# Kernel tuning notes

Measured on AMD Instinct MI355X. Metric: run time of the kernel, lower is better.

Reference implementation:

```python
import jax, jax.numpy as jnp
import numpy as np

B = 128; N_PER = 64; E_UND = 256
N_TOT = B * N_PER; E_DIR = 2 * B * E_UND; E_KEEP = B * E_UND
F_IN = 5; H1 = 256; H2 = 512; ATT = 3 * H2
EPS = 1e-5


def setup_inputs() -> dict:
    rng = np.random.default_rng(0)
    # undirected edges within each graph, stored in both directions
    u = rng.integers(0, N_PER, size=(B, E_UND))
    v = (u + rng.integers(1, N_PER, size=(B, E_UND))) % N_PER
    base = np.arange(B)[:, None] * N_PER
    lo = np.minimum(u, v) + base
    hi = np.maximum(u, v) + base
    edges = np.stack([np.concatenate([lo, hi], 1).reshape(-1),
                      np.concatenate([hi, lo], 1).reshape(-1)])
    ea = np.stack([rng.random(E_DIR).astype(np.float32),
                   rng.integers(0, 2, E_DIR).astype(np.float32)], axis=1)
    key = jax.random.key(0)
    ks = iter(jax.random.split(key, 16))
    lin = lambda i, o: jax.random.normal(next(ks), (i, o), jnp.float32) * 0.02
    return dict(
        x=jax.random.normal(next(ks), (N_TOT, F_IN), jnp.float32),
        edges=jnp.asarray(edges, jnp.int32),
        edge_attr=jnp.asarray(ea),
        detector_labels=jnp.ones((N_TOT,), bool),
        batch_labels=jnp.repeat(jnp.arange(B, dtype=jnp.int32), N_PER),
        w_emb_W=lin(3, 1), w_emb_b=jnp.zeros((1,), jnp.float32),
        gc1_Wrel=lin(F_IN, H1), gc1_brel=jnp.zeros((H1,)), gc1_Wroot=lin(F_IN, H1),
        gc2_Wrel=lin(H1, H2), gc2_brel=jnp.zeros((H2,)), gc2_Wroot=lin(H1, H2),
        gn_w=jnp.ones((H2,)), gn_b=jnp.zeros((H2,)), gn_ms=jnp.ones((H2,)),
        edge_emb_W=lin(3, H2), edge_emb_b=jnp.zeros((H2,)),
        qkv_W=lin(ATT, 3 * ATT), qkv_b=jnp.zeros((3 * ATT,)),
        in_Wq=lin(ATT, ATT), in_Wk=lin(ATT, ATT), in_Wv=lin(ATT, ATT),
        in_bq=jnp.zeros((ATT,)), in_bk=jnp.zeros((ATT,)), in_bv=jnp.zeros((ATT,)),
        out_W=lin(ATT, ATT), out_b=jnp.zeros((ATT,)),
        ln_g=jnp.ones((ATT,)), ln_b=jnp.zeros((ATT,)),
        head_W=lin(ATT, 1), head_b=jnp.zeros((1,)),
    )


def reference(x, edges, edge_attr, detector_labels, batch_labels,
              w_emb_W, w_emb_b, gc1_Wrel, gc1_brel, gc1_Wroot,
              gc2_Wrel, gc2_brel, gc2_Wroot, gn_w, gn_b, gn_ms,
              edge_emb_W, edge_emb_b, qkv_W, qkv_b,
              in_Wq, in_Wk, in_Wv, in_bq, in_bk, in_bv,
              out_W, out_b, ln_g, ln_b, head_W, head_b):
    src, dst = edges[0], edges[1]
    onehot = lambda c: jax.nn.one_hot(jax.lax.stop_gradient(c).astype(jnp.int32), 2, dtype=x.dtype)
    # edge-weight embedding
    w = jnp.concatenate([edge_attr[:, :1], onehot(edge_attr[:, 1])], axis=-1)
    w = jax.nn.relu(w @ w_emb_W + w_emb_b)  # [E_DIR, 1]

    def gconv(h, Wrel, brel, Wroot):  # torch_geometric GraphConv (aggr='add')
        agg = jax.ops.segment_sum(w * h[src], dst, num_segments=N_TOT)
        return jax.nn.relu(agg @ Wrel + brel + h @ Wroot)

    h = gconv(x, gc1_Wrel, gc1_brel, gc1_Wroot)
    h = gconv(h, gc2_Wrel, gc2_brel, gc2_Wroot)
    # GraphNorm: per-graph statistics
    cnt = jax.ops.segment_sum(jnp.ones((N_TOT, 1), h.dtype), batch_labels, num_segments=B)
    mean = jax.ops.segment_sum(h, batch_labels, num_segments=B) / cnt
    cen = h - gn_ms * mean[batch_labels]
    var = jax.ops.segment_sum(cen * cen, batch_labels, num_segments=B) / cnt
    h = gn_w * cen / jnp.sqrt(var + EPS)[batch_labels] + gn_b
    # SplitSyndromes: keep detector-detector edges with src > dst, then sort (row-major)
    keep = detector_labels[src] & detector_labels[dst] & (src > dst)
    kidx = jnp.nonzero(keep, size=E_KEEP)[0]  # E_KEEP known by construction
    e_src, e_dst, ea = src[kidx], dst[kidx], edge_attr[kidx]
    perm = jnp.argsort(e_src * N_TOT + e_dst)
    e_src, e_dst, ea = e_src[perm], e_dst[perm], ea[perm]
    emb = jax.nn.relu(jnp.concatenate([ea[:, :1], onehot(ea[:, 1])], -1) @ edge_emb_W + edge_emb_b)
    feat = jnp.concatenate([h[e_src], emb, h[e_dst]], axis=-1)  # [E_KEEP, ATT]
    # equal edge count per graph => unbatch + pad_sequence == reshape
    feat = feat.reshape(B, E_UND, ATT)
    se = e_src.reshape(B, E_UND); te = e_dst.reshape(B, E_UND)
    ec = ea[:, 1].reshape(B, E_UND, 1)
    mask = se == te  # key_padding_mask (all False: no padding here)
    # self-attention, 1 head
    q, k, v = jnp.split(feat @ qkv_W + qkv_b, 3, axis=-1)
    q = q @ in_Wq + in_bq; k = k @ in_Wk + in_bk; v = v @ in_Wv + in_bv
    scale = np.float32(1.0 / np.sqrt(ATT))
    scores = jnp.einsum('bqd,bkd->bqk', q, k) * scale
    scores = jnp.where(mask[:, None, :], -jnp.inf, scores)
    attn_out = jnp.einsum('bqk,bkd->bqd', jax.nn.softmax(scores, axis=-1), v) @ out_W + out_b
    feat = feat + attn_out
    mu = feat.mean(-1, keepdims=True)
    feat = ln_g * (feat - mu) * jax.lax.rsqrt(((feat - mu) ** 2).mean(-1, keepdims=True) + EPS) + ln_b
    out = feat @ head_W + head_b  # [B, E_UND, 1]
    pair = jnp.concatenate([out[:, ::2], out[:, 1::2]], axis=2)  # [B, E_UND/2, 2]
    ecp = jnp.concatenate([ec[:, ::2], ec[:, 1::2]], axis=2)
    min_inds = jnp.argmin(pair, axis=2, keepdims=True)
    val = jnp.take_along_axis(pair, min_inds, axis=2)
    cls = jnp.take_along_axis(ecp, min_inds, axis=2)
    edges_out = jnp.stack([se, te], axis=-1)[:, ::2, :]
    return edges_out, val, cls
```

## Files before the change

kernel.cpp:

```cpp
#include <hip/hip_runtime.h>
#include <math.h>

#define NTOT   8192
#define BGR    128
#define NPER   64
#define EDIR   65536
#define EKEEP  32768
#define EPSC   1e-5f

typedef unsigned short ushortT;
typedef __attribute__((ext_vector_type(8))) short bf16x8;
typedef __attribute__((ext_vector_type(4))) float f32x4;

#define C_BF 0
#define C_F32 1
#define C_RT 2

__device__ __forceinline__ float bf2f(ushortT u) {
    union { unsigned int i; float f; } v; v.i = ((unsigned int)u) << 16; return v.f;
}
__device__ __forceinline__ ushortT f2bf(float f) {
    unsigned int u = __float_as_uint(f);
    u += 0x7FFFu + ((u >> 16) & 1u);
    return (ushortT)(u >> 16);
}
__device__ __forceinline__ float get1(const void* p, long i, int f) {
    return f ? ((const float*)p)[i] : bf2f(((const ushortT*)p)[i]);
}
__device__ __forceinline__ float ld1c(const float* p)   { return *p; }
__device__ __forceinline__ float ld1c(const ushortT* p) { return bf2f(*p); }
__device__ __forceinline__ void st1c(float* p, float v)   { *p = v; }
__device__ __forceinline__ void st1c(ushortT* p, float v) { *p = f2bf(v); }
__device__ __forceinline__ int clampi(int v, int lo, int hi) {
    return v < lo ? lo : (v > hi ? hi : v);
}

__device__ __forceinline__ void gld16(const void* g, void* l) {
    __builtin_amdgcn_global_load_lds(
        (const __attribute__((address_space(1))) unsigned int*)g,
        (__attribute__((address_space(3))) unsigned int*)l, 16, 0, 0);
}

__device__ __forceinline__ int xcd_swz(int flat, int nwg) {
    const int q = nwg >> 3, r = nwg & 7;
    const int xcd = flat & 7, idx = flat >> 3;
    return (xcd < r ? xcd * (q + 1) : r * (q + 1) + (xcd - r) * q) + idx;
}

__launch_bounds__(256)
__global__ void detect_k(const unsigned int* __restrict__ xw, int* __restrict__ flag)
{
    __shared__ int red[256];
    const int t = threadIdx.x;
    int hits = 0;
#pragma unroll
    for (int i = 0; i < 4; ++i) {
        const unsigned w = xw[t*4 + i];
        const unsigned eb = (w >> 7) & 0xFF;
        hits += (eb >= 100 && eb <= 150) ? 1 : 0;
    }
    red[t] = hits; __syncthreads();
#pragma unroll
    for (int s = 128; s > 0; s >>= 1) { if (t < s) red[t] += red[t+s]; __syncthreads(); }
    if (t == 0) *flag = (red[0] < 512) ? 1 : 0;
}

template<class TC, bool BIAS, bool RESID, bool RELU>
__launch_bounds__(256)
__global__ void bgemm_k(const ushortT* __restrict__ A, const ushortT* __restrict__ B,
                        const float* __restrict__ bias, TC* __restrict__ C,
                        int K, int lda, int ldb, int ldc,
                        long sA, long sB, long sC, long biasOff, long bzStride,
                        float alpha)
{
    const int t = threadIdx.x;
    const int lane = t & 63, wave = t >> 6;
    const int l15 = lane & 15, quad = lane >> 4;
    const int wr = (wave >> 1) * 64, wc = (wave & 1) * 64;

    const int gx = gridDim.x, gy = gridDim.y;
    const int nwg = gx * gy * (int)gridDim.z;
    const int flat = xcd_swz(blockIdx.x + gx * (blockIdx.y + gy * blockIdx.z), nwg);
    const int bx = flat % gx;
    const int by = (flat / gx) % gy;
    const int bz = flat / (gx * gy);

    const int m0 = by * 128, n0 = bx * 128;
    const long z = bz;

    __shared__ __align__(16) ushortT As[128][64];
    __shared__ __align__(16) ushortT Bs[128][64];

    f32x4 acc[4][4] = {};

    const int sr = t >> 3;
    const int ssw = ((t & 7) ^ (sr & 7)) * 8;
    const ushortT* pA = A + z*sA + (long)(m0 + sr) * lda + ssw;
    const ushortT* pB = B + z*sB + (long)(n0 + sr) * ldb + ssw;
    ushortT* lA = &As[sr][(t & 7) * 8];
    ushortT* lB = &Bs[sr][(t & 7) * 8];

    for (int k0 = 0; k0 < K; k0 += 64) {
#pragma unroll
        for (int i = 0; i < 4; ++i) {
            gld16(pA + (long)i*32*lda + k0, lA + i*32*64);
            gld16(pB + (long)i*32*ldb + k0, lB + i*32*64);
        }
        __syncthreads();
#pragma unroll
        for (int kh = 0; kh < 2; ++kh) {
            const int ca = (kh*32 + quad*8) ^ ((l15 & 7) * 8);
            bf16x8 af[4], bfr[4];
#pragma unroll
            for (int i = 0; i < 4; ++i) {
                af[i]  = *(const bf16x8*)&As[wr + i*16 + l15][ca];
                bfr[i] = *(const bf16x8*)&Bs[wc + i*16 + l15][ca];
            }
#pragma unroll
            for (int mt = 0; mt < 4; ++mt)
#pragma unroll
                for (int nt = 0; nt < 4; ++nt)
                    acc[mt][nt] = __builtin_amdgcn_mfma_f32_16x16x32_bf16(af[mt], bfr[nt], acc[mt][nt], 0, 0, 0);
        }
        __syncthreads();
    }

    TC* Cb = C + z * sC;
#pragma unroll
    for (int nt = 0; nt < 4; ++nt) {
        const int col = n0 + wc + nt*16 + l15;
        const float bv = BIAS ? bias[biasOff + z*bzStride + col] : 0.f;
#pragma unroll
        for (int mt = 0; mt < 4; ++mt) {
#pragma unroll
            for (int r = 0; r < 4; ++r) {
                const int row = m0 + wr + mt*16 + quad*4 + r;
                TC* cp = Cb + (long)row * ldc + col;
                float val = alpha * acc[mt][nt][r] + bv;
                if constexpr (RESID) val += ld1c(cp);
                if constexpr (RELU)  val = fmaxf(val, 0.f);
                st1c(cp, val);
            }
        }
    }
}

__device__ __forceinline__ float blockReduceSum(float v, float* red, int t)
{
    red[t] = v; __syncthreads();
#pragma unroll
    for (int s = 128; s > 0; s >>= 1) {
        if (t < s) red[t] += red[t + s];
        __syncthreads();
    }
    const float r = red[0];
    __syncthreads();
    return r;
}

__launch_bounds__(256)
__global__ void convbf_k(const void* __restrict__ in, ushortT* __restrict__ out,
                         long n4, const int* __restrict__ flagp)
{
    const int f = *flagp;
    const long i = (long)blockIdx.x*256 + threadIdx.x;
    if (i >= n4) return;
    const long i0 = i * 4;
    if (f) {
        const float4 v = *(const float4*)((const float*)in + i0);
        ushort4 o; o.x=f2bf(v.x); o.y=f2bf(v.y); o.z=f2bf(v.z); o.w=f2bf(v.w);
        *(ushort4*)(out + i0) = o;
    } else {
        *(ushort4*)(out + i0) = *(const ushort4*)((const ushortT*)in + i0);
    }
}

__launch_bounds__(256)
__global__ void tconvbf_k(const void* __restrict__ in, ushortT* __restrict__ out,
                          const int* __restrict__ flagp)
{
    const int f = *flagp;
    __shared__ float tile[32][33];
    const int bx = blockIdx.x, by = blockIdx.y;
    const int tx = threadIdx.x & 31, ty = threadIdx.x >> 5;
#pragma unroll
    for (int i = 0; i < 4; ++i) {
        const int k = by*32 + ty + i*8;
        tile[ty + i*8][tx] = get1(in, (long)k*1536 + bx*32 + tx, f);
    }
    __syncthreads();
#pragma unroll
    for (int i = 0; i < 4; ++i) {
        const int n = bx*32 + ty + i*8;
        out[(long)n*1536 + by*32 + tx] = f2bf(tile[tx][ty + i*8]);
    }
}

__launch_bounds__(256)
__global__ void tconv512_k(const void* __restrict__ in, ushortT* __restrict__ out,
                           int koff, const int* __restrict__ flagp)
{
    const int f = *flagp;
    __shared__ float tile[32][33];
    const int bx = blockIdx.x, by = blockIdx.y;
    const int tx = threadIdx.x & 31, ty = threadIdx.x >> 5;
#pragma unroll
    for (int i = 0; i < 4; ++i) {
        const int k = by*32 + ty + i*8;
        tile[ty + i*8][tx] = get1(in, (long)k*512 + bx*32 + tx, f);
    }
    __syncthreads();
#pragma unroll
    for (int i = 0; i < 4; ++i) {
        const int n = bx*32 + ty + i*8;
        out[(long)n*512 + koff + by*32 + tx] = f2bf(tile[tx][ty + i*8]);
    }
}

__launch_bounds__(256)
__global__ void convf32_k(const void* __restrict__ in, float* __restrict__ out,
                          int n, const int* __restrict__ flagp)
{
    const int f = *flagp;
    const int i = blockIdx.x*256 + threadIdx.x;
    if (i < n) out[i] = get1(in, i, f);
}

__launch_bounds__(256)
__global__ void colcomb_part_k(const void* __restrict__ v, int cv, long voff,
                               const void* __restrict__ W, int cW,
                               float* __restrict__ part, const int* __restrict__ flagp)
{
    const int rtf = *flagp;
    const int fv = (cv == C_RT) ? rtf : cv;
    const int fW = (cW == C_RT) ? rtf : cW;
    const int d = blockIdx.x*256 + threadIdx.x;
    const int c0 = blockIdx.y * 24;
    float a = 0.f;
#pragma unroll
    for (int i = 0; i < 24; ++i) {
        const int c = c0 + i;
        a += get1(v, voff + c, fv) * get1(W, (long)c*1536 + d, fW);
    }
    part[blockIdx.y * 1536 + d] = a;
}

__launch_bounds__(256)
__global__ void colcomb_red_k(const float* __restrict__ part,
                              const void* __restrict__ b, int cb,
                              float* __restrict__ out, const int* __restrict__ flagp)
{
    const int rtf = *flagp;
    const int fb = (cb == C_RT) ? rtf : cb;
    const int d = blockIdx.x*256 + threadIdx.x;
    float a = get1(b, d, fb);
#pragma unroll 8
    for (int cy = 0; cy < 64; ++cy) a += part[cy*1536 + d];
    out[d] = a;
}

__launch_bounds__(256)
__global__ void rowdot_k(const ushortT* __restrict__ W, const float* __restrict__ v,
                         float* __restrict__ out, float scale)
{
    const int r = blockIdx.x, t = threadIdx.x;
    __shared__ float red[256];
    float p = 0.f;
    for (int c = t; c < 1536; c += 256) p += bf2f(W[(long)r*1536 + c]) * v[c];
    const float tot = blockReduceSum(p, red, t);
    if (t == 0) out[r] = scale * tot;
}

__launch_bounds__(256)
__global__ void gconv1_k(int b0, const void* __restrict__ x, const int* __restrict__ edges,
                         const void* __restrict__ ea,
                         const void* __restrict__ wembW, const void* __restrict__ wembB,
                         const void* __restrict__ Wrel, const void* __restrict__ brel,
                         const void* __restrict__ Wroot, ushortT* __restrict__ ah,
                         const int* __restrict__ flagp)
{
    const int f = *flagp;
    const int bl = blockIdx.x, g = b0 + bl, t = threadIdx.x;
    __shared__ float s_x[64][5];
    __shared__ float s_agg[64][5];
    __shared__ int   s_cnt[64];
    __shared__ int   s_off[65];
    __shared__ int   s_src[512];
    __shared__ float s_w[512];

    if (t < 64) s_cnt[t] = 0;
    if (t < 320) s_x[t/5][t%5] = get1(x, (long)(g*64 + t/5)*5 + (t%5), f);
    __syncthreads();

    const float w0 = get1(wembW,0,f), w1 = get1(wembW,1,f), w2 = get1(wembW,2,f);
    const float wb = get1(wembB,0,f);
    int sl[2], dl[2], slot[2]; float wv[2];
#pragma unroll
    for (int e2 = 0; e2 < 2; ++e2) {
        const int e = g*512 + t + 256*e2;
        const int s = edges[e], d = edges[EDIR + e];
        sl[e2] = clampi(s - g*64, 0, 63); dl[e2] = clampi(d - g*64, 0, 63);
        const float a0 = get1(ea, 2L*e, f), a1 = get1(ea, 2L*e+1, f);
        wv[e2] = fmaxf(a0*w0 + ((a1 < 0.5f) ? w1 : w2) + wb, 0.f);
        slot[e2] = atomicAdd(&s_cnt[dl[e2]], 1);
    }
    __syncthreads();
    if (t == 0) {
        int r = 0;
        for (int i = 0; i < 64; ++i) { s_off[i] = r; r += s_cnt[i]; }
        s_off[64] = r;
    }
    __syncthreads();
#pragma unroll
    for (int e2 = 0; e2 < 2; ++e2) {
        const int p = s_off[dl[e2]] + slot[e2];
        s_src[p] = sl[e2]; s_w[p] = wv[e2];
    }
    __syncthreads();
    if (t < 320) {
        const int n = t/5, k = t%5;
        float acc = 0.f;
        for (int i = s_off[n]; i < s_off[n+1]; ++i) acc += s_w[i] * s_x[s_src[i]][k];
        s_agg[n][k] = acc;
    }
    __syncthreads();
    float wr[5], wo[5];
#pragma unroll
    for (int k = 0; k < 5; ++k) { wr[k] = get1(Wrel, k*256 + t, f); wo[k] = get1(Wroot, k*256 + t, f); }
    const float bb = get1(brel, t, f);
    for (int n = 0; n < 64; ++n) {
        float v = bb;
#pragma unroll
        for (int k = 0; k < 5; ++k) v += s_agg[n][k]*wr[k] + s_x[n][k]*wo[k];
        ah[(long)(bl*64 + n)*512 + 256 + t] = f2bf(fmaxf(v, 0.f));
    }
}

__launch_bounds__(256)
__global__ void gconv2_agg_k(int b0, ushortT* __restrict__ ah, const int* __restrict__ edges,
                             const void* __restrict__ ea,
                             const void* __restrict__ wembW, const void* __restrict__ wembB,
                             const int* __restrict__ flagp)
{
    const int f = *flagp;
    const int bl = blockIdx.x, g = b0 + bl, t = threadIdx.x;
    __shared__ int   s_cnt[64];
    __shared__ int   s_off[65];
    __shared__ int   s_src[512];
    __shared__ float s_w[512];

    if (t < 64) s_cnt[t] = 0;
    __syncthreads();

    const float w0 = get1(wembW,0,f), w1 = get1(wembW,1,f), w2 = get1(wembW,2,f);
    const float wb = get1(wembB,0,f);
    int sl[2], dl[2], slot[2]; float wv[2];
#pragma unroll
    for (int e2 = 0; e2 < 2; ++e2) {
        const int e = g*512 + t + 256*e2;
        const int s = edges[e], d = edges[EDIR + e];
        sl[e2] = clampi(s - g*64, 0, 63); dl[e2] = clampi(d - g*64, 0, 63);
        const float a0 = get1(ea, 2L*e, f), a1 = get1(ea, 2L*e+1, f);
        wv[e2] = fmaxf(a0*w0 + ((a1 < 0.5f) ? w1 : w2) + wb, 0.f);
        slot[e2] = atomicAdd(&s_cnt[dl[e2]], 1);
    }
    __syncthreads();
    if (t == 0) {
        int r = 0;
        for (int i = 0; i < 64; ++i) { s_off[i] = r; r += s_cnt[i]; }
        s_off[64] = r;
    }
    __syncthreads();
#pragma unroll
    for (int e2 = 0; e2 < 2; ++e2) {
        const int p = s_off[dl[e2]] + slot[e2];
        s_src[p] = sl[e2]; s_w[p] = wv[e2];
    }
    __syncthreads();
    for (int n = 0; n < 64; ++n) {
        float acc = 0.f;
        const int i0 = s_off[n], i1 = s_off[n+1];
        for (int i = i0; i < i1; ++i)
            acc += s_w[i] * bf2f(ah[(long)(bl*64 + s_src[i])*512 + 256 + t]);
        ah[(long)(bl*64 + n)*512 + t] = f2bf(acc);
    }
}

__launch_bounds__(256)
__global__ void gnorm_k(ushortT* __restrict__ h, const void* __restrict__ gw,
                        const void* __restrict__ gb, const void* __restrict__ gms,
                        const int* __restrict__ flagp)
{
    const int f0 = *flagp;
    const int bl = blockIdx.x, t = threadIdx.x;
    const int f = t + 256*blockIdx.y;
    float acc = 0.f;
    for (int n = 0; n < 64; ++n) acc += bf2f(h[(bl*64+n)*512 + f]);
    const float m2 = get1(gms, f, f0) * (acc * (1.f/64.f));
    float v = 0.f;
    for (int n = 0; n < 64; ++n) { const float d = bf2f(h[(bl*64+n)*512 + f]) - m2; v += d*d; }
    const float rs = rsqrtf(v*(1.f/64.f) + EPSC);
    const float g = get1(gw, f, f0), bb = get1(gb, f, f0);
    for (int n = 0; n < 64; ++n) {
        const int idx = (bl*64+n)*512 + f;
        h[idx] = f2bf(g * (bf2f(h[idx]) - m2) * rs + bb);
    }
}

__launch_bounds__(256)
__global__ void sort_k(const int* __restrict__ edges, int* __restrict__ sorted_orig,
                       int* __restrict__ se, int* __restrict__ te)
{
    const int b = blockIdx.x, t = threadIdx.x;
    __shared__ int s_keep[512];
    __shared__ int s_key[512];
    __shared__ int s_ckey[256];
    __shared__ int s_corig[256];
#pragma unroll
    for (int e2 = 0; e2 < 2; ++e2) {
        const int el = t + 256*e2;
        const int e = b*512 + el;
        const int s = edges[e], d = edges[EDIR + e];
        s_keep[el] = (s > d) ? 1 : 0;
        s_key[el]  = ((s - b*64) << 6) | (d - b*64);
    }
    __syncthreads();
#pragma unroll
    for (int e2 = 0; e2 < 2; ++e2) {
        const int el = t + 256*e2;
        if (s_keep[el]) {
            int pos = 0;
            for (int j = 0; j < el; ++j) pos += s_keep[j];
            s_ckey[pos]  = s_key[el];
            s_corig[pos] = b*512 + el;
        }
    }
    __syncthreads();
    const int ki = s_ckey[t];
    int rank = 0;
    for (int j = 0; j < 256; ++j) {
        const int kj = s_ckey[j];
        rank += (kj < ki || (kj == ki && j < t)) ? 1 : 0;
    }
    const int orig = s_corig[t];
    const int p = b*256 + rank;
    sorted_orig[p] = orig;
    se[p] = edges[orig];
    te[p] = edges[EDIR + orig];
}

__launch_bounds__(256)
__global__ void fbuild_k(int b0, int maxn, const ushortT* __restrict__ h,
                         const int* __restrict__ sorted_orig,
                         const int* __restrict__ se, const int* __restrict__ te,
                         const void* __restrict__ ea,
                         const void* __restrict__ eW, const void* __restrict__ eB,
                         const float* __restrict__ kb,
                         ushortT* __restrict__ F, float* __restrict__ bvec,
                         const int* __restrict__ flagp)
{
    const int fl = *flagp;
    const int e = blockIdx.x, t = threadIdx.x;
    __shared__ float red[256];
    const int ge = b0*256 + e;
    const int s = clampi(se[ge] - b0*64, 0, maxn);
    const int d = clampi(te[ge] - b0*64, 0, maxn);
    const int orig = clampi(sorted_orig[ge], 0, EDIR-1);
    const float a0 = get1(ea, 2L*orig, fl), a1 = get1(ea, 2L*orig + 1, fl);
    float partial = 0.f;
#pragma unroll
    for (int c = 0; c < 6; ++c) {
        const int col = c*256 + t;
        float v;
        if (c < 2) {
            v = bf2f(h[(long)s*512 + col]);
        } else if (c < 4) {
            const int ff = col - 512;
            v = fmaxf(a0*get1(eW, ff, fl)
                      + ((a1 < 0.5f) ? get1(eW, 512+ff, fl) : get1(eW, 1024+ff, fl))
                      + get1(eB, ff, fl), 0.f);
        } else {
            v = bf2f(h[(long)d*512 + (col - 1024)]);
        }
        F[(long)e*1536 + col] = f2bf(v);
        partial += v * kb[col];
    }
    const float tot = blockReduceSum(partial, red, t);
    if (t == 0) bvec[ge] = tot;
}

__launch_bounds__(256)
__global__ void softmax_ip_k(float* __restrict__ S)
{
    const long row = blockIdx.x;
    const int t = threadIdx.x;
    __shared__ float red[256];
    const float v = S[row*256 + t];
    red[t] = v; __syncthreads();
#pragma unroll
    for (int s = 128; s > 0; s >>= 1) { if (t < s) red[t] = fmaxf(red[t], red[t+s]); __syncthreads(); }
    const float mx = red[0]; __syncthreads();
    const float e = __expf(v - mx);
    red[t] = e; __syncthreads();
#pragma unroll
    for (int s = 128; s > 0; s >>= 1) { if (t < s) red[t] += red[t+s]; __syncthreads(); }
    const float sum = red[0];
    ((ushortT*)S)[row*512 + t] = f2bf(e / sum);
}

__launch_bounds__(256)
__global__ void ln_head_k(int b0, const ushortT* __restrict__ F, const void* __restrict__ lng,
                          const void* __restrict__ lnb, const void* __restrict__ hW,
                          const void* __restrict__ hB, float* __restrict__ gout,
                          const int* __restrict__ flagp)
{
    const int fl = *flagp;
    const int e = blockIdx.x, t = threadIdx.x;
    __shared__ float red[256];
    float xv[6];
    float s = 0.f;
#pragma unroll
    for (int c = 0; c < 6; ++c) { xv[c] = bf2f(F[(long)e*1536 + c*256 + t]); s += xv[c]; }
    const float tot = blockReduceSum(s, red, t);
    const float mu = tot * (1.f/1536.f);
    float ss = 0.f;
#pragma unroll
    for (int c = 0; c < 6; ++c) { const float d = xv[c] - mu; ss += d*d; }
    const float tot2 = blockReduceSum(ss, red, t);
    const float rs = rsqrtf(tot2 * (1.f/1536.f) + EPSC);
    float p = 0.f;
#pragma unroll
    for (int c = 0; c < 6; ++c) {
        const int col = c*256 + t;
        p += (get1(lng, col, fl) * (xv[c] - mu) * rs + get1(lnb, col, fl)) * get1(hW, col, fl);
    }
    const float tot3 = blockReduceSum(p, red, t);
    if (t == 0) gout[b0*256 + e] = tot3 + get1(hB, 0, fl);
}

__launch_bounds__(128)
__global__ void final_k(const float* __restrict__ gout, const int* __restrict__ se,
                        const int* __restrict__ te, const int* __restrict__ sorted_orig,
                        const void* __restrict__ ea, float* __restrict__ out,
                        const int* __restrict__ flagp)
{
    const int fl = *flagp;
    const int b = blockIdx.x, j = threadIdx.x;
    const int e0 = b*256 + 2*j, e1 = e0 + 1;
    const float p0 = gout[e0], p1 = gout[e1];
    const int idx = (p1 < p0) ? 1 : 0;
    const float val = idx ? p1 : p0;
    const int eo = idx ? e1 : e0;
    const int orig = clampi(sorted_orig[eo], 0, EDIR-1);
    const float cls = get1(ea, 2L*orig + 1, fl);
    out[(b*128 + j)*2 + 0] = (float)se[e0];
    out[(b*128 + j)*2 + 1] = (float)te[e0];
    out[32768 + b*128 + j] = val;
    out[32768 + 16384 + b*128 + j] = cls;
}

extern "C" void kernel_launch(void* const* d_in, const int* in_sizes, int n_in,
                              void* d_out, int out_size, void* d_ws, size_t ws_size,
                              hipStream_t stream)
{
    (void)out_size;

    const void* x     = d_in[0];
    const int*  edges = (const int*)d_in[1];
    const void* ea    = d_in[2];

    int ws0 = 3;
    while (ws0 < n_in && in_sizes[ws0] != 3) ++ws0;
    if (ws0 + 27 > n_in) ws0 = 5;

    const void* wembW  = d_in[ws0 + 0];
    const void* wembB  = d_in[ws0 + 1];
    const void* g1Wrel = d_in[ws0 + 2];
    const void* g1brel = d_in[ws0 + 3];
    const void* g1Wroot= d_in[ws0 + 4];
    const void* g2Wrel = d_in[ws0 + 5];
    const void* g2brel = d_in[ws0 + 6];
    const void* g2Wroot= d_in[ws0 + 7];
    const void* gnw    = d_in[ws0 + 8];
    const void* gnb    = d_in[ws0 + 9];
    const void* gnms   = d_in[ws0 + 10];
    const void* eembW  = d_in[ws0 + 11];
    const void* eembB  = d_in[ws0 + 12];
    const void* qkvW   = d_in[ws0 + 13];
    const void* qkvb   = d_in[ws0 + 14];
    const void* inWq   = d_in[ws0 + 15];
    const void* inWk   = d_in[ws0 + 16];
    const void* inWv   = d_in[ws0 + 17];
    const void* inbq   = d_in[ws0 + 18];
    const void* inbv   = d_in[ws0 + 20];
    const void* outW   = d_in[ws0 + 21];
    const void* outb   = d_in[ws0 + 22];
    const void* lng    = d_in[ws0 + 23];
    const void* lnb    = d_in[ws0 + 24];
    const void* headW  = d_in[ws0 + 25];
    const void* headb  = d_in[ws0 + 26];

    char* ws = (char*)d_ws;
    size_t off = 0;
    auto alloc = [&](size_t bytes) {
        void* p = ws + off;
        off = (off + bytes + 255) & ~(size_t)255;
        return p;
    };
    int*     dflag  = (int*)    alloc(256);
    float*   gout   = (float*)  alloc(EKEEP*4);
    int*     sorted = (int*)    alloc(EKEEP*4);
    int*     seg    = (int*)    alloc(EKEEP*4);
    int*     teg    = (int*)    alloc(EKEEP*4);
    float*   bvec   = (float*)  alloc(EKEEP*4);
    float*   bqc    = (float*)  alloc(1536*4);
    float*   bvc    = (float*)  alloc(1536*4);
    float*   kb     = (float*)  alloc(1536*4);
    float*   bvo    = (float*)  alloc(1536*4);
    float*   g2bf   = (float*)  alloc(512*4);
    float*   colpart= (float*)  alloc(64L*1536*4);
    ushortT* Wg2T   = (ushortT*)alloc(512L*512*2);
    ushortT* MpWv   = (ushortT*)alloc(2L*1536*1536*2);
    ushortT* MpT    = MpWv;
    ushortT* Wvo    = MpWv + 1536L*1536;
    const size_t fixedB = off;

    const long W2 = 1536L * 1536;
    ushortT* Wqc    = (ushortT*)(ws + fixedB);
    ushortT* Wkc    = Wqc + W2;
    ushortT* Wvc    = Wqc + 2*W2;
    ushortT* outWT  = Wqc + 3*W2;
    ushortT* qkvWbf = Wqc + 4*W2;
    ushortT* inWqT  = Wqc + 7*W2;
    ushortT* inWkT  = Wqc + 8*W2;
    ushortT* inWvT  = Wqc + 9*W2;

    const size_t perG = 64L*512*2 + 64L*512*2 + 2L*256*1536*2 + 256L*256*4;
    int G = 128;
    while (G > 2 && fixedB + (size_t)G*perG + 65536 > ws_size) G >>= 1;

    size_t coff = fixedB;
    auto calloc2 = [&](size_t bytes) {
        void* p = ws + coff;
        coff = (coff + bytes + 255) & ~(size_t)255;
        return p;
    };
    ushortT* h_c  = (ushortT*)calloc2((size_t)G*64*512*2);
    ushortT* ah_c = (ushortT*)calloc2((size_t)G*64*512*2);
    ushortT* F_c  = (ushortT*)calloc2((size_t)G*256*1536*2);
    ushortT* T_c  = (ushortT*)calloc2((size_t)G*256*1536*2);
    float*   S_c  = (float*)  calloc2((size_t)G*256*256*4);

    const float scale = 0.02551551815399144f;
    const dim3 blk(256);

    detect_k<<<1, blk, 0, stream>>>((const unsigned int*)x, dflag);
    sort_k<<<128, blk, 0, stream>>>(edges, sorted, seg, teg);

    convbf_k<<<(1536*4608/4 + 255)/256, blk, 0, stream>>>(qkvW, qkvWbf, 1536L*4608/4, dflag);
    tconvbf_k<<<dim3(48,48), blk, 0, stream>>>(inWq, inWqT, dflag);
    tconvbf_k<<<dim3(48,48), blk, 0, stream>>>(inWk, inWkT, dflag);
    tconvbf_k<<<dim3(48,48), blk, 0, stream>>>(inWv, inWvT, dflag);
    tconvbf_k<<<dim3(48,48), blk, 0, stream>>>(outW, outWT, dflag);
    tconv512_k<<<dim3(16,8), blk, 0, stream>>>(g2Wrel, Wg2T, 0, dflag);
    tconv512_k<<<dim3(16,8), blk, 0, stream>>>(g2Wroot, Wg2T, 256, dflag);
    convf32_k<<<2, blk, 0, stream>>>(g2brel, g2bf, 512, dflag);
    bgemm_k<ushortT,false,false,false><<<dim3(12,12,3), blk, 0, stream>>>(
        qkvWbf, inWqT, nullptr, Wqc, 1536, 4608, 1536, 1536,
        1536L, W2, W2, 0, 0, 1.f);
    colcomb_part_k<<<dim3(6,64), blk, 0, stream>>>(qkvb, C_RT, 0, inWq, C_RT, colpart, dflag);
    colcomb_red_k<<<6, blk, 0, stream>>>(colpart, inbq, C_RT, bqc, dflag);
    rowdot_k<<<1536, blk, 0, stream>>>(Wkc, bqc, kb, scale);
    colcomb_part_k<<<dim3(6,64), blk, 0, stream>>>(qkvb, C_RT, 3072, inWv, C_RT, colpart, dflag);
    colcomb_red_k<<<6, blk, 0, stream>>>(colpart, inbv, C_RT, bvc, dflag);
    bgemm_k<ushortT,false,false,false><<<dim3(12,12,2), blk, 0, stream>>>(
        Wkc, Wqc, nullptr, MpT, 1536, 1536, 1536, 1536,
        W2, 3*W2, W2, 0, 0, 1.f);
    colcomb_part_k<<<dim3(6,64), blk, 0, stream>>>(bvc, C_F32, 0, outW, C_RT, colpart, dflag);
    colcomb_red_k<<<6, blk, 0, stream>>>(colpart, outb, C_RT, bvo, dflag);

    const int nchunk = 128 / G;
    const int EC = G * 256;
    for (int c = 0; c < nchunk; ++c) {
        const int b0 = c * G;
        const int maxn = G*64 - 1;
        gconv1_k<<<G, blk, 0, stream>>>(b0, x, edges, ea, wembW, wembB,
                                        g1Wrel, g1brel, g1Wroot, ah_c, dflag);
        gconv2_agg_k<<<G, blk, 0, stream>>>(b0, ah_c, edges, ea, wembW, wembB, dflag);
        bgemm_k<ushortT,true,false,true><<<dim3(4, G/2, 1), blk, 0, stream>>>(
            ah_c, Wg2T, g2bf, h_c, 512, 512, 512, 512, 0,0,0, 0, 0, 1.f);
        gnorm_k<<<dim3(G,2), blk, 0, stream>>>(h_c, gnw, gnb, gnms, dflag);
        fbuild_k<<<EC, blk, 0, stream>>>(b0, maxn, h_c, sorted, seg, teg, ea,
                                         eembW, eembB, kb, F_c, bvec, dflag);
        bgemm_k<ushortT,false,false,false><<<dim3(12, EC/128, 1), blk, 0, stream>>>(
            F_c, MpT, nullptr, T_c, 1536, 1536, 1536, 1536, 0,0,0, 0,0, 1.f);
        bgemm_k<float,true,false,false><<<dim3(2, 2, G), blk, 0, stream>>>(
            T_c, F_c, bvec + (long)b0*256, S_c, 1536, 1536, 1536, 256,
            256L*1536, 256L*1536, 65536L, 0, 256, scale);
        softmax_ip_k<<<EC, blk, 0, stream>>>(S_c);
        bgemm_k<ushortT,false,false,false><<<dim3(2, 12, G), blk, 0, stream>>>(
            Wvo, F_c, nullptr, T_c, 1536, 1536, 1536, 256,
            0L, 256L*1536, 256L*1536, 0, 0, 1.f);
        bgemm_k<ushortT,true,true,false><<<dim3(12, 2, G), blk, 0, stream>>>(
            (const ushortT*)S_c, T_c, bvo, F_c, 256, 512, 256, 1536,
            131072L, 256L*1536, 256L*1536, 0, 0, 1.f);
        ln_head_k<<<EC, blk, 0, stream>>>(b0, F_c, lng, lnb, headW, headb, gout, dflag);
    }

    final_k<<<128, dim3(128), 0, stream>>>(gout, seg, teg, sorted, ea, (float*)d_out, dflag);
}
```

Baseline: 1.025 ms.

## Fuse score GEMM with softmax, merge transposes, split graph-conv blocks, vectorize LN

Adds a score-GEMM kernel that computes a 64-row by 256-column tile per block and applies the bias, row max, exp and normalisation in registers. It writes the bf16 probabilities directly, so the separate softmax kernel and its fp32 round trip through memory go away. It also folds the four weight-transpose launches into one z-indexed launch and splits each graph-conv kernel across two blocks per graph to raise parallelism. The LN/head kernel now reads 8 bf16 values per thread with vector loads. The fused kernel launches only 4 blocks per graph and holds a large shared B tile, which may hurt occupancy, and the split graph-conv blocks duplicate the edge sorting work.

Measured after the change: 1.158 ms. +12.9%, slower.

```diff
diff --git a/kernel.cpp b/kernel.cpp
--- a/kernel.cpp
+++ b/kernel.cpp
@@ -141,6 +141,118 @@
                 if constexpr (RELU)  val = fmaxf(val, 0.f);
                 st1c(cp, val);
             }
+        }
+    }
+}
+
+__launch_bounds__(256)
+__global__ void sgemm_sm_k(const ushortT* __restrict__ A, const ushortT* __restrict__ B,
+                           const float* __restrict__ bvec, float* __restrict__ S,
+                           float alpha)
+{
+    const int t = threadIdx.x;
+    const int lane = t & 63, wave = t >> 6;
+    const int l15 = lane & 15, quad = lane >> 4;
+
+    const int gx = gridDim.x;
+    const int nwg = gx * (int)gridDim.y;
+    const int flat = xcd_swz(blockIdx.x + gx * blockIdx.y, nwg);
+    const int rb = flat % gx;
+    const int z  = flat / gx;
+
+    const int m0 = rb * 64;
+
+    __shared__ __align__(16) ushortT As[64][64];
+    __shared__ __align__(16) ushortT Bs[256][64];
+    __shared__ float redA[4][64];
+    __shared__ float redB[4][64];
+
+    f32x4 acc[4][4] = {};
+
+    const int sr = t >> 3;
+    const int ssw = ((t & 7) ^ (sr & 7)) * 8;
+    const ushortT* pA = A + (long)z*256*1536 + (long)(m0 + sr) * 1536 + ssw;
+    const ushortT* pB = B + (long)z*256*1536 + (long)sr * 1536 + ssw;
+    ushortT* lA = &As[sr][(t & 7) * 8];
+    ushortT* lB = &Bs[sr][(t & 7) * 8];
+
+    for (int k0 = 0; k0 < 1536; k0 += 64) {
+        gld16(pA + k0, lA);
+        gld16(pA + 32L*1536 + k0, lA + 32*64);
+#pragma unroll
+        for (int i = 0; i < 8; ++i)
+            gld16(pB + (long)i*32*1536 + k0, lB + i*32*64);
+        __syncthreads();
+#pragma unroll
+        for (int kh = 0; kh < 2; ++kh) {
+            const int ca = (kh*32 + quad*8) ^ ((l15 & 7) * 8);
+            bf16x8 af[4], bfr[4];
+#pragma unroll
+            for (int i = 0; i < 4; ++i) {
+                af[i]  = *(const bf16x8*)&As[i*16 + l15][ca];
+                bfr[i] = *(const bf16x8*)&Bs[wave*64 + i*16 + l15][ca];
+            }
+#pragma unroll
+            for (int mt = 0; mt < 4; ++mt)
+#pragma unroll
+                for (int nt = 0; nt < 4; ++nt)
+                    acc[mt][nt] = __builtin_amdgcn_mfma_f32_16x16x32_bf16(af[mt], bfr[nt], acc[mt][nt], 0, 0, 0);
+        }
+        __syncthreads();
+    }
+
+    float bv[4];
+#pragma unroll
+    for (int nt = 0; nt < 4; ++nt)
+        bv[nt] = bvec[z*256 + wave*64 + nt*16 + l15];
+
+#pragma unroll
+    for (int mt = 0; mt < 4; ++mt) {
+#pragma unroll
+        for (int r = 0; r < 4; ++r) {
+            float m = -3.4e38f;
+#pragma unroll
+            for (int nt = 0; nt < 4; ++nt)
+                m = fmaxf(m, alpha * acc[mt][nt][r] + bv[nt]);
+#pragma unroll
+            for (int sh = 1; sh < 16; sh <<= 1)
+                m = fmaxf(m, __shfl_xor(m, sh));
+            if (l15 == 0) redA[wave][mt*16 + quad*4 + r] = m;
+        }
+    }
+    __syncthreads();
+#pragma unroll
+    for (int mt = 0; mt < 4; ++mt) {
+#pragma unroll
+        for (int r = 0; r < 4; ++r) {
+            const int lr = mt*16 + quad*4 + r;
+            const float mx = fmaxf(fmaxf(redA[0][lr], redA[1][lr]),
+                                   fmaxf(redA[2][lr], redA[3][lr]));
+            float s = 0.f;
+#pragma unroll
+            for (int nt = 0; nt < 4; ++nt) {
+                const float e = __expf(alpha * acc[mt][nt][r] + bv[nt] - mx);
+                acc[mt][nt][r] = e;
+                s += e;
+            }
+#pragma unroll
+            for (int sh = 1; sh < 16; sh <<= 1)
+                s += __shfl_xor(s, sh);
+            if (l15 == 0) redB[wave][lr] = s;
+        }
+    }
+    __syncthreads();
+    ushortT* P = (ushortT*)S + (long)z*131072 + (long)m0*512;
+#pragma unroll
+    for (int mt = 0; mt < 4; ++mt) {
+#pragma unroll
+        for (int r = 0; r < 4; ++r) {
+            const int lr = mt*16 + quad*4 + r;
+            const float den = redB[0][lr] + redB[1][lr] + redB[2][lr] + redB[3][lr];
+            const float inv = 1.f / den;
+#pragma unroll
+            for (int nt = 0; nt < 4; ++nt)
+                P[(long)lr*512 + wave*64 + nt*16 + l15] = f2bf(acc[mt][nt][r] * inv);
         }
     }
 }
@@ -176,10 +288,20 @@
 }
 
 __launch_bounds__(256)
-__global__ void tconvbf_k(const void* __restrict__ in, ushortT* __restrict__ out,
-                          const int* __restrict__ flagp)
+__global__ void tconvbf4_k(const void* __restrict__ i0, const void* __restrict__ i1,
+                           const void* __restrict__ i2, const void* __restrict__ i3,
+                           ushortT* __restrict__ o0, ushortT* __restrict__ o1,
+                           ushortT* __restrict__ o2, ushortT* __restrict__ o3,
+                           const int* __restrict__ flagp)
 {
     const int f = *flagp;
+    const void* in; ushortT* out;
+    switch (blockIdx.z) {
+        case 0:  in = i0; out = o0; break;
+        case 1:  in = i1; out = o1; break;
+        case 2:  in = i2; out = o2; break;
+        default: in = i3; out = o3; break;
+    }
     __shared__ float tile[32][33];
     const int bx = blockIdx.x, by = blockIdx.y;
     const int tx = threadIdx.x & 31, ty = threadIdx.x >> 5;
@@ -281,6 +403,7 @@
 {
     const int f = *flagp;
     const int bl = blockIdx.x, g = b0 + bl, t = threadIdx.x;
+    const int nb0 = blockIdx.y * 32;
     __shared__ float s_x[64][5];
     __shared__ float s_agg[64][5];
     __shared__ int   s_cnt[64];
@@ -317,8 +440,8 @@
         s_src[p] = sl[e2]; s_w[p] = wv[e2];
     }
     __syncthreads();
-    if (t < 320) {
-        const int n = t/5, k = t%5;
+    if (t < 160) {
+        const int n = nb0 + t/5, k = t%5;
         float acc = 0.f;
         for (int i = s_off[n]; i < s_off[n+1]; ++i) acc += s_w[i] * s_x[s_src[i]][k];
         s_agg[n][k] = acc;
@@ -328,7 +451,7 @@
 #pragma unroll
     for (int k = 0; k < 5; ++k) { wr[k] = get1(Wrel, k*256 + t, f); wo[k] = get1(Wroot, k*256 + t, f); }
     const float bb = get1(brel, t, f);
-    for (int n = 0; n < 64; ++n) {
+    for (int n = nb0; n < nb0 + 32; ++n) {
         float v = bb;
 #pragma unroll
         for (int k = 0; k < 5; ++k) v += s_agg[n][k]*wr[k] + s_x[n][k]*wo[k];
@@ -344,6 +467,7 @@
 {
     const int f = *flagp;
     const int bl = blockIdx.x, g = b0 + bl, t = threadIdx.x;
+    const int nb0 = blockIdx.y * 32;
     __shared__ int   s_cnt[64];
     __shared__ int   s_off[65];
     __shared__ int   s_src[512];
@@ -377,7 +501,7 @@
         s_src[p] = sl[e2]; s_w[p] = wv[e2];
     }
     __syncthreads();
-    for (int n = 0; n < 64; ++n) {
+    for (int n = nb0; n < nb0 + 32; ++n) {
         float acc = 0.f;
         const int i0 = s_off[n], i1 = s_off[n+1];
         for (int i = i0; i < i1; ++i)
@@ -490,25 +614,6 @@
 }
 
 __launch_bounds__(256)
-__global__ void softmax_ip_k(float* __restrict__ S)
-{
-    const long row = blockIdx.x;
-    const int t = threadIdx.x;
-    __shared__ float red[256];
-    const float v = S[row*256 + t];
-    red[t] = v; __syncthreads();
-#pragma unroll
-    for (int s = 128; s > 0; s >>= 1) { if (t < s) red[t] = fmaxf(red[t], red[t+s]); __syncthreads(); }
-    const float mx = red[0]; __syncthreads();
-    const float e = __expf(v - mx);
-    red[t] = e; __syncthreads();
-#pragma unroll
-    for (int s = 128; s > 0; s >>= 1) { if (t < s) red[t] += red[t+s]; __syncthreads(); }
-    const float sum = red[0];
-    ((ushortT*)S)[row*512 + t] = f2bf(e / sum);
-}
-
-__launch_bounds__(256)
 __global__ void ln_head_k(int b0, const ushortT* __restrict__ F, const void* __restrict__ lng,
                           const void* __restrict__ lnb, const void* __restrict__ hW,
                           const void* __restrict__ hB, float* __restrict__ gout,
@@ -517,22 +622,33 @@
     const int fl = *flagp;
     const int e = blockIdx.x, t = threadIdx.x;
     __shared__ float red[256];
-    float xv[6];
+    const bool act = t < 192;
+    float xv[8];
     float s = 0.f;
-#pragma unroll
-    for (int c = 0; c < 6; ++c) { xv[c] = bf2f(F[(long)e*1536 + c*256 + t]); s += xv[c]; }
+    if (act) {
+        const bf16x8 v = *(const bf16x8*)&F[(long)e*1536 + t*8];
+#pragma unroll
+        for (int j = 0; j < 8; ++j) { xv[j] = bf2f((ushortT)v[j]); s += xv[j]; }
+    } else {
+#pragma unroll
+        for (int j = 0; j < 8; ++j) xv[j] = 0.f;
+    }
     const float tot = blockReduceSum(s, red, t);
     const float mu = tot * (1.f/1536.f);
     float ss = 0.f;
-#pragma unroll
-    for (int c = 0; c < 6; ++c) { const float d = xv[c] - mu; ss += d*d; }
+    if (act) {
+#pragma unroll
+        for (int j = 0; j < 8; ++j) { const float d = xv[j] - mu; ss += d*d; }
+    }
     const float tot2 = blockReduceSum(ss, red, t);
     const float rs = rsqrtf(tot2 * (1.f/1536.f) + EPSC);
     float p = 0.f;
-#pragma unroll
-    for (int c = 0; c < 6; ++c) {
-        const int col = c*256 + t;
-        p += (get1(lng, col, fl) * (xv[c] - mu) * rs + get1(lnb, col, fl)) * get1(hW, col, fl);
+    if (act) {
+#pragma unroll
+        for (int j = 0; j < 8; ++j) {
+            const int col = t*8 + j;
+            p += (get1(lng, col, fl) * (xv[j] - mu) * rs + get1(lnb, col, fl)) * get1(hW, col, fl);
+        }
     }
     const float tot3 = blockReduceSum(p, red, t);
     if (t == 0) gout[b0*256 + e] = tot3 + get1(hB, 0, fl);
@@ -658,10 +774,8 @@
     sort_k<<<128, blk, 0, stream>>>(edges, sorted, seg, teg);
 
     convbf_k<<<(1536*4608/4 + 255)/256, blk, 0, stream>>>(qkvW, qkvWbf, 1536L*4608/4, dflag);
-    tconvbf_k<<<dim3(48,48), blk, 0, stream>>>(inWq, inWqT, dflag);
-    tconvbf_k<<<dim3(48,48), blk, 0, stream>>>(inWk, inWkT, dflag);
-    tconvbf_k<<<dim3(48,48), blk, 0, stream>>>(inWv, inWvT, dflag);
-    tconvbf_k<<<dim3(48,48), blk, 0, stream>>>(outW, outWT, dflag);
+    tconvbf4_k<<<dim3(48,48,4), blk, 0, stream>>>(inWq, inWk, inWv, outW,
+                                                  inWqT, inWkT, inWvT, outWT, dflag);
     tconv512_k<<<dim3(16,8), blk, 0, stream>>>(g2Wrel, Wg2T, 0, dflag);
     tconv512_k<<<dim3(16,8), blk, 0, stream>>>(g2Wroot, Wg2T, 256, dflag);
     convf32_k<<<2, blk, 0, stream>>>(g2brel, g2bf, 512, dflag);
@@ -684,9 +798,9 @@
     for (int c = 0; c < nchunk; ++c) {
         const int b0 = c * G;
         const int maxn = G*64 - 1;
-        gconv1_k<<<G, blk, 0, stream>>>(b0, x, edges, ea, wembW, wembB,
-                                        g1Wrel, g1brel, g1Wroot, ah_c, dflag);
-        gconv2_agg_k<<<G, blk, 0, stream>>>(b0, ah_c, edges, ea, wembW, wembB, dflag);
+        gconv1_k<<<dim3(G,2), blk, 0, stream>>>(b0, x, edges, ea, wembW, wembB,
+                                                g1Wrel, g1brel, g1Wroot, ah_c, dflag);
+        gconv2_agg_k<<<dim3(G,2), blk, 0, stream>>>(b0, ah_c, edges, ea, wembW, wembB, dflag);
         bgemm_k<ushortT,true,false,true><<<dim3(4, G/2, 1), blk, 0, stream>>>(
             ah_c, Wg2T, g2bf, h_c, 512, 512, 512, 512, 0,0,0, 0, 0, 1.f);
         gnorm_k<<<dim3(G,2), blk, 0, stream>>>(h_c, gnw, gnb, gnms, dflag);
@@ -694,10 +808,8 @@
                                          eembW, eembB, kb, F_c, bvec, dflag);
         bgemm_k<ushortT,false,false,false><<<dim3(12, EC/128, 1), blk, 0, stream>>>(
             F_c, MpT, nullptr, T_c, 1536, 1536, 1536, 1536, 0,0,0, 0,0, 1.f);
-        bgemm_k<float,true,false,false><<<dim3(2, 2, G), blk, 0, stream>>>(
-            T_c, F_c, bvec + (long)b0*256, S_c, 1536, 1536, 1536, 256,
-            256L*1536, 256L*1536, 65536L, 0, 256, scale);
-        softmax_ip_k<<<EC, blk, 0, stream>>>(S_c);
+        sgemm_sm_k<<<dim3(4, G), blk, 0, stream>>>(
+            T_c, F_c, bvec + (long)b0*256, S_c, scale);
         bgemm_k<ushortT,false,false,false><<<dim3(2, 12, G), blk, 0, stream>>>(
             Wvo, F_c, nullptr, T_c, 1536, 1536, 1536, 256,
             0L, 256L*1536, 256L*1536, 0, 0, 1.f);
```
